# Performance work log

Measured on AMD Instinct MI355X. Metric: run time of the kernel, lower is better.

The kernel has to match this reference:

```python
import jax, jax.numpy as jnp
import numpy as np


def setup_inputs() -> dict:
    key = jax.random.key(0)
    k1, k2, k3, k4 = jax.random.split(key, 4)
    B, C, T = 32, 512, 1024
    N, D = 64, 512
    scale = 1.0 / np.sqrt(C)
    x = jax.random.normal(k1, (B, C, T), dtype=jnp.float32)
    subjects = jax.random.randint(k2, (B,), 0, N, dtype=jnp.int64)
    weights = jax.random.normal(k3, (N, C, D), dtype=jnp.float32) * scale
    bias = jax.random.normal(k4, (N, D), dtype=jnp.float32) * scale
    return {"x": x, "subjects": subjects, "weights": weights, "bias": bias}


def reference(x, subjects, weights, bias):
    # gather mode: per-example projection matrix, then batched GEMM
    # x: (B, C, T); weights[subjects]: (B, C, D) -> out: (B, D, T)
    w = weights[subjects]                      # (B, C, D)
    out = jnp.einsum('bct,bcd->bdt', x, w)
    out = out + bias[subjects][:, :, None]     # (B, D, 1) broadcast over T
    return out
```

## Files before the change

kernel.cpp:

```cpp
#include <hip/hip_runtime.h>
#include <hip/hip_bf16.h>

#define B_N 32
#define C_K 512
#define T_N 1024
#define D_M 512

constexpr int BM = 128, BN = 128, BK = 32;
constexpr int SA = 36;
constexpr int KSTEPS = C_K / BK;

typedef __attribute__((ext_vector_type(4))) float  floatx4;
typedef __attribute__((ext_vector_type(4))) short  shortx4;
typedef __attribute__((ext_vector_type(8))) short  shortx8;
typedef __attribute__((ext_vector_type(2))) unsigned int uintx2;

__device__ __forceinline__ unsigned pk2(float a, float b) {
  __hip_bfloat162 h = __float22bfloat162_rn(make_float2(a, b));
  union { __hip_bfloat162 v; unsigned u; } c; c.v = h; return c.u;
}

__global__ __launch_bounds__(256, 3)
void subject_gemm(const float* __restrict__ x, const int* __restrict__ subjects,
                  const float* __restrict__ weights, const float* __restrict__ bias,
                  float* __restrict__ out)
{
  __shared__ short lds_a[2][BM * SA];
  __shared__ short lds_b[2][BN * SA];

  const int bid  = blockIdx.x;
  const int xcd  = bid & 7;
  const int s    = bid >> 3;
  const int b    = xcd * 4 + (s & 3);
  const int tile = s >> 2;
  const int tm = tile >> 3, tn = tile & 7;
  const int m0 = tm * BM, n0 = tn * BN;
  const int nb = subjects[b];

  const float* __restrict__ Wp = weights + (size_t)nb * C_K * D_M;
  const float* __restrict__ Xp = x + (size_t)b * C_K * T_N;

  const int tid  = threadIdx.x;
  const int lane = tid & 63;
  const int wave = tid >> 6;

  const bool isA = (wave < 2);
  const int  mg  = (wave & 1) * 16 + (lane & 15);
  const int  oct = lane >> 4;
  const float* gsrc = isA ? (Wp + (size_t)(8 * oct) * D_M + (m0 + 4 * mg))
                          : (Xp + (size_t)(8 * oct) * T_N + (n0 + 4 * mg));
  const int gs = isA ? D_M : T_N;
  short* const wbase = (isA ? &lds_a[0][0] : &lds_b[0][0]) + (4 * mg) * SA + 8 * oct;
  constexpr int BUFO = BM * SA;

  const int wm = (wave & 1) * 64, wn = (wave >> 1) * 64;
  const int l15 = lane & 15, q = lane >> 4;

  floatx4 acc[4][4] = {};
  floatx4 v[8];

  #pragma unroll
  for (int jj = 0; jj < 8; ++jj)
    v[jj] = *(const floatx4*)(gsrc + (size_t)jj * gs);
  gsrc += (size_t)BK * gs;
  #pragma unroll
  for (int r = 0; r < 4; ++r) {
    uintx2 lo = { pk2(v[0][r], v[1][r]), pk2(v[2][r], v[3][r]) };
    uintx2 hi = { pk2(v[4][r], v[5][r]), pk2(v[6][r], v[7][r]) };
    *(uintx2*)(wbase + r * SA)     = lo;
    *(uintx2*)(wbase + r * SA + 4) = hi;
  }

  for (int ks = 0; ks < KSTEPS; ++ks) {
    const int p = ks & 1;
    __syncthreads();

    if (ks + 1 < KSTEPS) {
      #pragma unroll
      for (int jj = 0; jj < 8; ++jj)
        v[jj] = *(const floatx4*)(gsrc + (size_t)jj * gs);
      gsrc += (size_t)BK * gs;
    }

    const short* pa = &lds_a[p][0] + (wm + l15) * SA + 8 * q;
    const short* pb = &lds_b[p][0] + (wn + l15) * SA + 8 * q;
    shortx8 af[4], bg[4];
    #pragma unroll
    for (int i = 0; i < 4; ++i) {
      shortx4 alo = *(const shortx4*)(pa + 16 * i * SA);
      shortx4 ahi = *(const shortx4*)(pa + 16 * i * SA + 4);
      shortx4 blo = *(const shortx4*)(pb + 16 * i * SA);
      shortx4 bhi = *(const shortx4*)(pb + 16 * i * SA + 4);
      af[i] = __builtin_shufflevector(alo, ahi, 0, 1, 2, 3, 4, 5, 6, 7);
      bg[i] = __builtin_shufflevector(blo, bhi, 0, 1, 2, 3, 4, 5, 6, 7);
    }
    #pragma unroll
    for (int i = 0; i < 4; ++i)
      #pragma unroll
      for (int j = 0; j < 4; ++j)
        acc[i][j] = __builtin_amdgcn_mfma_f32_16x16x32_bf16(af[i], bg[j], acc[i][j], 0, 0, 0);

    if (ks + 1 < KSTEPS) {
      short* wdst = wbase + (p ^ 1) * BUFO;
      #pragma unroll
      for (int r = 0; r < 4; ++r) {
        uintx2 lo = { pk2(v[0][r], v[1][r]), pk2(v[2][r], v[3][r]) };
        uintx2 hi = { pk2(v[4][r], v[5][r]), pk2(v[6][r], v[7][r]) };
        *(uintx2*)(wdst + r * SA)     = lo;
        *(uintx2*)(wdst + r * SA + 4) = hi;
      }
    }
  }

  float* __restrict__ O = out + (size_t)b * D_M * T_N;
  const float* __restrict__ bb = bias + (size_t)nb * D_M;
  #pragma unroll
  for (int i = 0; i < 4; ++i) {
    #pragma unroll
    for (int r = 0; r < 4; ++r) {
      const int d = m0 + wm + 16 * i + 4 * q + r;
      const float bv = bb[d];
      #pragma unroll
      for (int j = 0; j < 4; ++j) {
        const int t = n0 + wn + 16 * j + l15;
        O[(size_t)d * T_N + t] = acc[i][j][r] + bv;
      }
    }
  }
}

extern "C" void kernel_launch(void* const* d_in, const int* in_sizes, int n_in,
                              void* d_out, int out_size, void* d_ws, size_t ws_size,
                              hipStream_t stream) {
  const float* x        = (const float*)d_in[0];
  const int*   subjects = (const int*)d_in[1];
  const float* weights  = (const float*)d_in[2];
  const float* bias     = (const float*)d_in[3];
  float* out = (float*)d_out;
  (void)in_sizes; (void)n_in; (void)out_size; (void)d_ws; (void)ws_size;

  dim3 grid(B_N * 4 * 8);
  dim3 block(256);
  hipLaunchKernelGGL(subject_gemm, grid, block, 0, stream, x, subjects, weights, bias, out);
}
```

Baseline: 180.3 us.

## Deepen global prefetch to two stages and widen LDS accesses to 128-bit

Restructures the K loop into a 2x-unrolled pipeline with two register sets so global loads for step k+2 are in flight while step k computes. It pads LDS rows to 40 shorts so staging writes and fragment reads become single 16-byte accesses, and remaps lanes so each thread packs a full 8-element row chunk. The __syncthreads is replaced by an inline waitcnt+barrier, and the bias is loaded as a vector in the epilogue. The extra register set raises VGPR pressure against the 3-blocks-per-SIMD launch bound, which could cause spills or lower occupancy.

```diff
diff --git a/kernel.cpp b/kernel.cpp
--- a/kernel.cpp
+++ b/kernel.cpp
@@ -7,17 +7,44 @@
 #define D_M 512
 
 constexpr int BM = 128, BN = 128, BK = 32;
-constexpr int SA = 36;
+constexpr int SA = 40;
 constexpr int KSTEPS = C_K / BK;
 
-typedef __attribute__((ext_vector_type(4))) float  floatx4;
-typedef __attribute__((ext_vector_type(4))) short  shortx4;
-typedef __attribute__((ext_vector_type(8))) short  shortx8;
-typedef __attribute__((ext_vector_type(2))) unsigned int uintx2;
+typedef __attribute__((ext_vector_type(4))) float floatx4;
+typedef __attribute__((ext_vector_type(8))) short shortx8;
+typedef __attribute__((ext_vector_type(4))) unsigned int uintx4;
 
 __device__ __forceinline__ unsigned pk2(float a, float b) {
   __hip_bfloat162 h = __float22bfloat162_rn(make_float2(a, b));
   union { __hip_bfloat162 v; unsigned u; } c; c.v = h; return c.u;
+}
+
+__device__ __forceinline__ void lds_barrier() {
+  asm volatile("s_waitcnt lgkmcnt(0)\n\ts_barrier" ::: "memory");
+}
+
+__device__ __forceinline__ void stage(const floatx4* v, short* dst) {
+  #pragma unroll
+  for (int r = 0; r < 4; ++r) {
+    uintx4 pkv = { pk2(v[0][r], v[1][r]), pk2(v[2][r], v[3][r]),
+                   pk2(v[4][r], v[5][r]), pk2(v[6][r], v[7][r]) };
+    *(uintx4*)(dst + r * SA) = pkv;
+  }
+}
+
+__device__ __forceinline__ void mfma_step(const short* pa, const short* pb,
+                                          floatx4 (&acc)[4][4]) {
+  shortx8 af[4], bg[4];
+  #pragma unroll
+  for (int i = 0; i < 4; ++i) {
+    af[i] = *(const shortx8*)(pa + 16 * i * SA);
+    bg[i] = *(const shortx8*)(pb + 16 * i * SA);
+  }
+  #pragma unroll
+  for (int i = 0; i < 4; ++i)
+    #pragma unroll
+    for (int j = 0; j < 4; ++j)
+      acc[i][j] = __builtin_amdgcn_mfma_f32_16x16x32_bf16(af[i], bg[j], acc[i][j], 0, 0, 0);
 }
 
 __global__ __launch_bounds__(256, 3)
@@ -45,85 +72,64 @@
   const int wave = tid >> 6;
 
   const bool isA = (wave < 2);
-  const int  mg  = (wave & 1) * 16 + (lane & 15);
-  const int  oct = lane >> 4;
-  const float* gsrc = isA ? (Wp + (size_t)(8 * oct) * D_M + (m0 + 4 * mg))
-                          : (Xp + (size_t)(8 * oct) * T_N + (n0 + 4 * mg));
+  const int  mgg = (wave & 1) * 16 + (lane >> 2);
+  const int  oct = lane & 3;
+  const float* gsrc = isA ? (Wp + (size_t)(8 * oct) * D_M + (m0 + 4 * mgg))
+                          : (Xp + (size_t)(8 * oct) * T_N + (n0 + 4 * mgg));
   const int gs = isA ? D_M : T_N;
-  short* const wbase = (isA ? &lds_a[0][0] : &lds_b[0][0]) + (4 * mg) * SA + 8 * oct;
-  constexpr int BUFO = BM * SA;
+  short* const wb0 = (isA ? lds_a[0] : lds_b[0]) + (4 * mgg) * SA + 8 * oct;
+  short* const wb1 = (isA ? lds_a[1] : lds_b[1]) + (4 * mgg) * SA + 8 * oct;
+  const size_t gstep = (size_t)BK * gs;
 
   const int wm = (wave & 1) * 64, wn = (wave >> 1) * 64;
   const int l15 = lane & 15, q = lane >> 4;
+  const short* pa0 = lds_a[0] + (wm + l15) * SA + 8 * q;
+  const short* pb0 = lds_b[0] + (wn + l15) * SA + 8 * q;
+  const short* pa1 = lds_a[1] + (wm + l15) * SA + 8 * q;
+  const short* pb1 = lds_b[1] + (wn + l15) * SA + 8 * q;
 
   floatx4 acc[4][4] = {};
-  floatx4 v[8];
+  floatx4 u[8], w[8];
 
   #pragma unroll
-  for (int jj = 0; jj < 8; ++jj)
-    v[jj] = *(const floatx4*)(gsrc + (size_t)jj * gs);
-  gsrc += (size_t)BK * gs;
+  for (int jj = 0; jj < 8; ++jj) u[jj] = *(const floatx4*)(gsrc + (size_t)jj * gs);
+  stage(u, wb0);
   #pragma unroll
-  for (int r = 0; r < 4; ++r) {
-    uintx2 lo = { pk2(v[0][r], v[1][r]), pk2(v[2][r], v[3][r]) };
-    uintx2 hi = { pk2(v[4][r], v[5][r]), pk2(v[6][r], v[7][r]) };
-    *(uintx2*)(wbase + r * SA)     = lo;
-    *(uintx2*)(wbase + r * SA + 4) = hi;
-  }
+  for (int jj = 0; jj < 8; ++jj) w[jj] = *(const floatx4*)(gsrc + gstep + (size_t)jj * gs);
+  const float* gnext = gsrc + 2 * gstep;
 
-  for (int ks = 0; ks < KSTEPS; ++ks) {
-    const int p = ks & 1;
-    __syncthreads();
+  for (int ks = 0; ks < KSTEPS; ks += 2) {
+    lds_barrier();
+    if (ks + 2 < KSTEPS) {
+      #pragma unroll
+      for (int jj = 0; jj < 8; ++jj) u[jj] = *(const floatx4*)(gnext + (size_t)jj * gs);
+      gnext += gstep;
+    }
+    mfma_step(pa0, pb0, acc);
+    stage(w, wb1);
 
-    if (ks + 1 < KSTEPS) {
+    lds_barrier();
+    if (ks + 3 < KSTEPS) {
       #pragma unroll
-      for (int jj = 0; jj < 8; ++jj)
-        v[jj] = *(const floatx4*)(gsrc + (size_t)jj * gs);
-      gsrc += (size_t)BK * gs;
+      for (int jj = 0; jj < 8; ++jj) w[jj] = *(const floatx4*)(gnext + (size_t)jj * gs);
+      gnext += gstep;
     }
-
-    const short* pa = &lds_a[p][0] + (wm + l15) * SA + 8 * q;
-    const short* pb = &lds_b[p][0] + (wn + l15) * SA + 8 * q;
-    shortx8 af[4], bg[4];
-    #pragma unroll
-    for (int i = 0; i < 4; ++i) {
-      shortx4 alo = *(const shortx4*)(pa + 16 * i * SA);
-      shortx4 ahi = *(const shortx4*)(pa + 16 * i * SA + 4);
-      shortx4 blo = *(const shortx4*)(pb + 16 * i * SA);
-      shortx4 bhi = *(const shortx4*)(pb + 16 * i * SA + 4);
-      af[i] = __builtin_shufflevector(alo, ahi, 0, 1, 2, 3, 4, 5, 6, 7);
-      bg[i] = __builtin_shufflevector(blo, bhi, 0, 1, 2, 3, 4, 5, 6, 7);
-    }
-    #pragma unroll
-    for (int i = 0; i < 4; ++i)
-      #pragma unroll
-      for (int j = 0; j < 4; ++j)
-        acc[i][j] = __builtin_amdgcn_mfma_f32_16x16x32_bf16(af[i], bg[j], acc[i][j], 0, 0, 0);
-
-    if (ks + 1 < KSTEPS) {
-      short* wdst = wbase + (p ^ 1) * BUFO;
-      #pragma unroll
-      for (int r = 0; r < 4; ++r) {
-        uintx2 lo = { pk2(v[0][r], v[1][r]), pk2(v[2][r], v[3][r]) };
-        uintx2 hi = { pk2(v[4][r], v[5][r]), pk2(v[6][r], v[7][r]) };
-        *(uintx2*)(wdst + r * SA)     = lo;
-        *(uintx2*)(wdst + r * SA + 4) = hi;
-      }
-    }
+    mfma_step(pa1, pb1, acc);
+    if (ks + 2 < KSTEPS) stage(u, wb0);
   }
 
   float* __restrict__ O = out + (size_t)b * D_M * T_N;
   const float* __restrict__ bb = bias + (size_t)nb * D_M;
   #pragma unroll
   for (int i = 0; i < 4; ++i) {
+    const floatx4 bv = *(const floatx4*)(bb + m0 + wm + 16 * i + 4 * q);
     #pragma unroll
     for (int r = 0; r < 4; ++r) {
       const int d = m0 + wm + 16 * i + 4 * q + r;
-      const float bv = bb[d];
       #pragma unroll
       for (int j = 0; j < 4; ++j) {
         const int t = n0 + wn + 16 * j + l15;
-        O[(size_t)d * T_N + t] = acc[i][j][r] + bv;
+        O[(size_t)d * T_N + t] = acc[i][j][r] + bv[r];
       }
     }
   }
```

After: 218.3 us. +21.1%, slower.
